# Optimization experiments

Hardware: AMD Instinct MI355X
Metric: run time of the kernel (lower is better)

Reference implementation:

```python
import jax, jax.numpy as jnp
import numpy as np

B, E, C, K, H, OUT = 8192, 16, 256, 2, 64, 387

def setup_inputs() -> dict:
    ks = jax.random.split(jax.random.key(0), 6)
    x = jax.random.normal(ks[0], (B, E, C), dtype=jnp.float32)
    adj = jax.random.normal(ks[1], (E, E), dtype=jnp.float32) * (6.0 / (E + E)) ** 0.5  # xavier-ish
    adj_bias = jax.random.normal(ks[2], (1,), dtype=jnp.float32) * 0.1
    cheb_w = jax.random.normal(ks[3], (K * C, H), dtype=jnp.float32) * (6.0 / (K * C + H)) ** 0.5
    brelu_bias = jnp.zeros((1, 1, H), dtype=jnp.float32)
    fc_w = jax.random.normal(ks[4], (OUT, H), dtype=jnp.float32) * (1.0 / H) ** 0.5
    fc_b = jax.random.normal(ks[5], (OUT,), dtype=jnp.float32) * (1.0 / H) ** 0.5
    return {"x": x, "adj": adj, "adj_bias": adj_bias, "cheb_w": cheb_w,
            "brelu_bias": brelu_bias, "fc_w": fc_w, "fc_b": fc_b}

def reference(x, adj, adj_bias, cheb_w, brelu_bias, fc_w, fc_b):
    # adaptive adjacency + biased ReLU (Eq. 4 prelude)
    w = jax.nn.relu(adj + adj_bias)  # (E,E)
    # normalized Laplacian: I - D^{-1/2} W D^{-1/2}
    d_re = 1.0 / jnp.sqrt(jnp.sum(w, axis=1) + 1e-5)  # (E,)
    lap = jnp.eye(E, dtype=x.dtype) - d_re[:, None] * w * d_re[None, :]  # (E,E)
    # Chebyshev polynomial, k=2: T0 = ones, T1 = lap @ x
    t0 = jnp.ones_like(x)                       # (B,E,C)
    t1 = jnp.einsum('ij,bjc->bic', lap, x)      # (B,E,C)
    # torch: stack on dim=1 -> permute(0,2,3,1) -> flatten(2)  == interleave along last axis
    cp = jnp.stack([t0, t1], axis=-1).reshape(B, E, K * C)  # (B,E,K*C)
    h = jnp.einsum('bek,kh->beh', cp, cheb_w)   # (B,E,H)
    # dropout is identity at eval
    h = jax.nn.relu(brelu_bias + h)
    out = jnp.einsum('beh,oh->beo', h, fc_w) + fc_b  # (B,E,OUT)
    return out
```

## Files before the change

kernel.cpp:

```cpp
#include <hip/hip_runtime.h>
#include <stdint.h>


typedef __attribute__((ext_vector_type(4))) float f32x4;
typedef __attribute__((ext_vector_type(8))) short s16x8;
typedef __attribute__((ext_vector_type(4))) short s16x4;

#define WS_CH_B    0
#define WS_LAP_B   256
#define WS_LAPA_B  1280
#define WS_FCB_B   1792
#define WS_W1T2_B  4096
#define WS_FCW2_B  36864

static __device__ __forceinline__ short f2bf(float f) {
    union { float f; uint32_t u; } v; v.f = f;
    uint32_t r = (v.u + 0x7fffu + ((v.u >> 16) & 1u)) >> 16;
    return (short)r;
}

__global__ void prep_kernel(const float* __restrict__ adj,
                            const float* __restrict__ adj_bias,
                            const float* __restrict__ cheb_w,
                            const float* __restrict__ brelu_bias,
                            const float* __restrict__ fc_w,
                            const float* __restrict__ fc_b,
                            char* __restrict__ ws) {
    float* chf  = (float*)(ws + WS_CH_B);
    float* lapf = (float*)(ws + WS_LAP_B);
    short* lapA = (short*)(ws + WS_LAPA_B);
    float* fcbp = (float*)(ws + WS_FCB_B);
    short* w1t2 = (short*)(ws + WS_W1T2_B);
    short* fcw2 = (short*)(ws + WS_FCW2_B);
    int t = threadIdx.x;

    if (blockIdx.x == 0) {
        __shared__ float sw[16][17];
        __shared__ float sdre[16];
        __shared__ float slap[16][16];
        __shared__ float csum[4][64];
        float ab = adj_bias[0];
        {
            int i = t >> 4, j = t & 15;
            sw[i][j] = fmaxf(adj[t] + ab, 0.f);
        }
        {
            int hh = t & 63, part = t >> 6;
            float s = 0.f;
            #pragma unroll 8
            for (int i = 0; i < 64; ++i) s += cheb_w[(2 * (part * 64 + i)) * 64 + hh];
            csum[part][hh] = s;
        }
        __syncthreads();
        if (t < 16) {
            float s = 0.f;
            #pragma unroll
            for (int j = 0; j < 16; ++j) s += sw[t][j];
            sdre[t] = 1.0f / sqrtf(s + 1e-5f);
        }
        __syncthreads();
        {
            int i = t >> 4, j = t & 15;
            float l = (i == j ? 1.f : 0.f) - sdre[i] * sw[i][j] * sdre[j];
            slap[i][j] = l;
            lapf[t] = l;
        }
        __syncthreads();
        if (t < 64) {
            int m = t & 15, qq = t >> 4;
            #pragma unroll
            for (int i = 0; i < 4; ++i)
                lapA[t * 4 + i] = f2bf(slap[m][qq * 4 + i]);
            chf[t] = csum[0][t] + csum[1][t] + csum[2][t] + csum[3][t] + brelu_bias[t];
        }
        for (int o = t; o < 400; o += 256) fcbp[o] = (o < 387) ? fc_b[o] : 0.f;
    }
    int gt = blockIdx.x * blockDim.x + t;
    int nthr = gridDim.x * blockDim.x;
    for (int idx = gt; idx < 32 * 512; idx += nthr) {
        int frag = idx >> 9, r = idx & 511;
        int lane = r >> 3, j = r & 7;
        int kb = frag >> 2, nt = frag & 3;
        int k = kb * 32 + (lane >> 4) * 8 + j;
        int col = nt * 16 + (lane & 15);
        w1t2[idx] = f2bf(cheb_w[(2 * k + 1) * 64 + col]);
    }
    for (int idx = gt; idx < 50 * 512; idx += nthr) {
        int frag = idx >> 9, r = idx & 511;
        int lane = r >> 3, j = r & 7;
        int tt = frag >> 1, f = frag & 1;
        int o = tt * 16 + (lane & 15);
        int k = f * 32 + (lane >> 4) * 8 + j;
        fcw2[idx] = (o < 387) ? f2bf(fc_w[o * 64 + k]) : (short)0;
    }
}

__global__ __launch_bounds__(256) void fused_kernel(
        const float* __restrict__ x,
        const char* __restrict__ ws,
        float* __restrict__ out) {
    const float* chf  = (const float*)(ws + WS_CH_B);
    const short* lapA = (const short*)(ws + WS_LAPA_B);
    const float* fcbp = (const float*)(ws + WS_FCB_B);
    const short* w1t2 = (const short*)(ws + WS_W1T2_B);
    const short* fcw2 = (const short*)(ws + WS_FCW2_B);

    __shared__ __align__(16) short hs[4][16][72];

    const int lane = threadIdx.x & 63;
    const int wave = threadIdx.x >> 6;
    const int n = lane & 15;
    const int q = lane >> 4;
    const long b = (long)blockIdx.x * 4 + wave;

    const float* xrow = x + b * 4096 + n * 256 + q * 8;
    f32x4 xr[16];
    #pragma unroll
    for (int kb = 0; kb < 8; ++kb) {
        xr[2 * kb]     = *(const f32x4*)(xrow + kb * 32);
        xr[2 * kb + 1] = *(const f32x4*)(xrow + kb * 32 + 4);
    }
    s16x8 af[8];
    #pragma unroll
    for (int kb = 0; kb < 8; ++kb) {
        f32x4 xa = xr[2 * kb], xc = xr[2 * kb + 1];
        af[kb][0] = f2bf(xa[0]); af[kb][1] = f2bf(xa[1]);
        af[kb][2] = f2bf(xa[2]); af[kb][3] = f2bf(xa[3]);
        af[kb][4] = f2bf(xc[0]); af[kb][5] = f2bf(xc[1]);
        af[kb][6] = f2bf(xc[2]); af[kb][7] = f2bf(xc[3]);
    }
    const short* w1 = w1t2 + lane * 8;
    s16x8 bfr[2][4];
    #pragma unroll
    for (int nt = 0; nt < 4; ++nt)
        bfr[0][nt] = *(const s16x8*)(w1 + nt * 512);
    f32x4 g[4];
    #pragma unroll
    for (int nt = 0; nt < 4; ++nt) g[nt] = (f32x4){0.f, 0.f, 0.f, 0.f};
    #pragma unroll
    for (int kb = 0; kb < 8; ++kb) {
        const int cur = kb & 1;
        if (kb < 7) {
            #pragma unroll
            for (int nt = 0; nt < 4; ++nt)
                bfr[cur ^ 1][nt] = *(const s16x8*)(w1 + ((kb + 1) * 4 + nt) * 512);
        }
        #pragma unroll
        for (int nt = 0; nt < 4; ++nt)
            g[nt] = __builtin_amdgcn_mfma_f32_16x16x32_bf16(af[kb], bfr[cur][nt], g[nt], 0, 0, 0);
    }

    f32x4 h[4];
#if defined(__has_builtin) && __has_builtin(__builtin_amdgcn_mfma_f32_16x16x16bf16_1k)
    {
        s16x4 la = *(const s16x4*)(lapA + lane * 4);
        const f32x4 z4 = (f32x4){0.f, 0.f, 0.f, 0.f};
        #pragma unroll
        for (int nt = 0; nt < 4; ++nt) {
            s16x4 gb;
            gb[0] = f2bf(g[nt][0]); gb[1] = f2bf(g[nt][1]);
            gb[2] = f2bf(g[nt][2]); gb[3] = f2bf(g[nt][3]);
            h[nt] = __builtin_amdgcn_mfma_f32_16x16x16bf16_1k(la, gb, z4, 0, 0, 0);
        }
    }
#else
    {
        __shared__ float gs[4][16][68];
        const float* lapf = (const float*)(ws + WS_LAP_B);
        #pragma unroll
        for (int r = 0; r < 4; ++r) {
            gs[wave][q * 4 + r][0 * 16 + n] = g[0][r];
            gs[wave][q * 4 + r][1 * 16 + n] = g[1][r];
            gs[wave][q * 4 + r][2 * 16 + n] = g[2][r];
            gs[wave][q * 4 + r][3 * 16 + n] = g[3][r];
        }
        __syncthreads();
        #pragma unroll
        for (int nt = 0; nt < 4; ++nt) h[nt] = (f32x4){0.f, 0.f, 0.f, 0.f};
        #pragma unroll
        for (int e = 0; e < 16; ++e) {
            float l0 = lapf[(q * 4 + 0) * 16 + e];
            float l1 = lapf[(q * 4 + 1) * 16 + e];
            float l2 = lapf[(q * 4 + 2) * 16 + e];
            float l3 = lapf[(q * 4 + 3) * 16 + e];
            #pragma unroll
            for (int nt = 0; nt < 4; ++nt) {
                float gv = gs[wave][e][nt * 16 + n];
                h[nt][0] += l0 * gv; h[nt][1] += l1 * gv;
                h[nt][2] += l2 * gv; h[nt][3] += l3 * gv;
            }
        }
    }
#endif

    #pragma unroll
    for (int nt = 0; nt < 4; ++nt) {
        float cv = chf[nt * 16 + n];
        #pragma unroll
        for (int r = 0; r < 4; ++r) {
            float v = fmaxf(h[nt][r] + cv, 0.f);
            hs[wave][q * 4 + r][nt * 16 + n] = f2bf(v);
        }
    }
    __builtin_amdgcn_s_waitcnt(0xC07F);

    const short* fw = fcw2 + lane * 8;
    s16x8 fb[2][10];
    #pragma unroll
    for (int t = 0; t < 5; ++t) {
        fb[0][2 * t]     = *(const s16x8*)(fw + (t * 2 + 0) * 512);
        fb[0][2 * t + 1] = *(const s16x8*)(fw + (t * 2 + 1) * 512);
    }
    s16x8 ha0 = *(const s16x8*)(&hs[wave][n][q * 8]);
    s16x8 ha1 = *(const s16x8*)(&hs[wave][n][32 + q * 8]);
    float* outb = out + (b * 16 + q * 4) * 387;
    #pragma unroll
    for (int c = 0; c < 5; ++c) {
        if (c < 4) {
            #pragma unroll
            for (int t = 0; t < 5; ++t) {
                int tt = (c + 1) * 5 + t;
                fb[(c + 1) & 1][2 * t]     = *(const s16x8*)(fw + (tt * 2 + 0) * 512);
                fb[(c + 1) & 1][2 * t + 1] = *(const s16x8*)(fw + (tt * 2 + 1) * 512);
            }
        }
        #pragma unroll
        for (int t = 0; t < 5; ++t) {
            const int tt = c * 5 + t;
            const int o = tt * 16 + n;
            float bias = fcbp[o];
            f32x4 acc = (f32x4){bias, bias, bias, bias};
            acc = __builtin_amdgcn_mfma_f32_16x16x32_bf16(ha0, fb[c & 1][2 * t], acc, 0, 0, 0);
            acc = __builtin_amdgcn_mfma_f32_16x16x32_bf16(ha1, fb[c & 1][2 * t + 1], acc, 0, 0, 0);
            if (o < 387) {
                outb[0 * 387 + o] = acc[0];
                outb[1 * 387 + o] = acc[1];
                outb[2 * 387 + o] = acc[2];
                outb[3 * 387 + o] = acc[3];
            }
        }
    }
}

extern "C" void kernel_launch(void* const* d_in, const int* in_sizes, int n_in,
                              void* d_out, int out_size, void* d_ws, size_t ws_size,
                              hipStream_t stream) {
    const float* x          = (const float*)d_in[0];
    const float* adj        = (const float*)d_in[1];
    const float* adj_bias   = (const float*)d_in[2];
    const float* cheb_w     = (const float*)d_in[3];
    const float* brelu_bias = (const float*)d_in[4];
    const float* fc_w       = (const float*)d_in[5];
    const float* fc_b       = (const float*)d_in[6];
    float* outp = (float*)d_out;
    char* ws = (char*)d_ws;

    prep_kernel<<<64, 256, 0, stream>>>(adj, adj_bias, cheb_w, brelu_bias, fc_w, fc_b, ws);
    fused_kernel<<<2048, 256, 0, stream>>>(x, ws, outp);
}
```

Measured before the change: 345.1 us.

## Stage cheb weights in LDS and split FC output tiles across waves

At the start of the block, the cheb weight fragments (32KB) are copied into shared memory, and the first GEMM reads its B operands from LDS instead of global/L2. The FC stage is also re-partitioned. Each wave now loads only its own subset of output-column tiles of fc_w and applies them to all four waves' hidden rows, which are shared through LDS after a barrier. This cuts per-wave fc_w loads by roughly 4x, at the cost of a block-wide barrier, about 32KB more LDS per block (lower occupancy), and load imbalance because 25 tiles are spread over 4 waves.

Measured after the change: 343.0 us. No clear change (-0.6%).

```diff
diff --git a/kernel.cpp b/kernel.cpp
--- a/kernel.cpp
+++ b/kernel.cpp
@@ -105,13 +105,22 @@
     const short* w1t2 = (const short*)(ws + WS_W1T2_B);
     const short* fcw2 = (const short*)(ws + WS_FCW2_B);
 
-    __shared__ __align__(16) short hs[4][16][72];
+    __shared__ __align__(16) short sw1[32 * 512];
+    __shared__ __align__(16) short hs[4][16][80];
 
     const int lane = threadIdx.x & 63;
     const int wave = threadIdx.x >> 6;
     const int n = lane & 15;
     const int q = lane >> 4;
     const long b = (long)blockIdx.x * 4 + wave;
+
+    {
+        const s16x8* srcv = (const s16x8*)w1t2;
+        s16x8* dstv = (s16x8*)sw1;
+        #pragma unroll
+        for (int i = 0; i < 8; ++i)
+            dstv[i * 256 + threadIdx.x] = srcv[i * 256 + threadIdx.x];
+    }
 
     const float* xrow = x + b * 4096 + n * 256 + q * 8;
     f32x4 xr[16];
@@ -129,11 +138,13 @@
         af[kb][4] = f2bf(xc[0]); af[kb][5] = f2bf(xc[1]);
         af[kb][6] = f2bf(xc[2]); af[kb][7] = f2bf(xc[3]);
     }
-    const short* w1 = w1t2 + lane * 8;
+    __syncthreads();
+
+    const short* w1l = sw1 + lane * 8;
     s16x8 bfr[2][4];
     #pragma unroll
     for (int nt = 0; nt < 4; ++nt)
-        bfr[0][nt] = *(const s16x8*)(w1 + nt * 512);
+        bfr[0][nt] = *(const s16x8*)(w1l + nt * 512);
     f32x4 g[4];
     #pragma unroll
     for (int nt = 0; nt < 4; ++nt) g[nt] = (f32x4){0.f, 0.f, 0.f, 0.f};
@@ -143,7 +154,7 @@
         if (kb < 7) {
             #pragma unroll
             for (int nt = 0; nt < 4; ++nt)
-                bfr[cur ^ 1][nt] = *(const s16x8*)(w1 + ((kb + 1) * 4 + nt) * 512);
+                bfr[cur ^ 1][nt] = *(const s16x8*)(w1l + ((kb + 1) * 4 + nt) * 512);
         }
         #pragma unroll
         for (int nt = 0; nt < 4; ++nt)
@@ -202,37 +213,45 @@
             hs[wave][q * 4 + r][nt * 16 + n] = f2bf(v);
         }
     }
-    __builtin_amdgcn_s_waitcnt(0xC07F);
 
     const short* fw = fcw2 + lane * 8;
-    s16x8 fb[2][10];
-    #pragma unroll
-    for (int t = 0; t < 5; ++t) {
-        fb[0][2 * t]     = *(const s16x8*)(fw + (t * 2 + 0) * 512);
-        fb[0][2 * t + 1] = *(const s16x8*)(fw + (t * 2 + 1) * 512);
-    }
-    s16x8 ha0 = *(const s16x8*)(&hs[wave][n][q * 8]);
-    s16x8 ha1 = *(const s16x8*)(&hs[wave][n][32 + q * 8]);
-    float* outb = out + (b * 16 + q * 4) * 387;
-    #pragma unroll
-    for (int c = 0; c < 5; ++c) {
-        if (c < 4) {
-            #pragma unroll
-            for (int t = 0; t < 5; ++t) {
-                int tt = (c + 1) * 5 + t;
-                fb[(c + 1) & 1][2 * t]     = *(const s16x8*)(fw + (tt * 2 + 0) * 512);
-                fb[(c + 1) & 1][2 * t + 1] = *(const s16x8*)(fw + (tt * 2 + 1) * 512);
-            }
-        }
-        #pragma unroll
-        for (int t = 0; t < 5; ++t) {
-            const int tt = c * 5 + t;
-            const int o = tt * 16 + n;
-            float bias = fcbp[o];
+    s16x8 fb[2][2];
+    {
+        const int tt0 = wave;
+        fb[0][0] = *(const s16x8*)(fw + (tt0 * 2 + 0) * 512);
+        fb[0][1] = *(const s16x8*)(fw + (tt0 * 2 + 1) * 512);
+    }
+    asm volatile("s_waitcnt lgkmcnt(0)" ::: "memory");
+    __builtin_amdgcn_s_barrier();
+    __builtin_amdgcn_sched_barrier(0);
+
+    s16x8 ha[4][2];
+    #pragma unroll
+    for (int gi = 0; gi < 4; ++gi) {
+        ha[gi][0] = *(const s16x8*)(&hs[gi][n][q * 8]);
+        ha[gi][1] = *(const s16x8*)(&hs[gi][n][32 + q * 8]);
+    }
+
+    const long bbase = (long)blockIdx.x * 4;
+    #pragma unroll
+    for (int i = 0; i < 7; ++i) {
+        const int tt = wave + 4 * i;
+        if (tt >= 25) break;
+        const int cur = i & 1;
+        const int tn = tt + 4;
+        if (tn < 25) {
+            fb[cur ^ 1][0] = *(const s16x8*)(fw + (tn * 2 + 0) * 512);
+            fb[cur ^ 1][1] = *(const s16x8*)(fw + (tn * 2 + 1) * 512);
+        }
+        const int o = tt * 16 + n;
+        const float bias = fcbp[o];
+        #pragma unroll
+        for (int gi = 0; gi < 4; ++gi) {
             f32x4 acc = (f32x4){bias, bias, bias, bias};
-            acc = __builtin_amdgcn_mfma_f32_16x16x32_bf16(ha0, fb[c & 1][2 * t], acc, 0, 0, 0);
-            acc = __builtin_amdgcn_mfma_f32_16x16x32_bf16(ha1, fb[c & 1][2 * t + 1], acc, 0, 0, 0);
+            acc = __builtin_amdgcn_mfma_f32_16x16x32_bf16(ha[gi][0], fb[cur][0], acc, 0, 0, 0);
+            acc = __builtin_amdgcn_mfma_f32_16x16x32_bf16(ha[gi][1], fb[cur][1], acc, 0, 0, 0);
             if (o < 387) {
+                float* outb = out + ((bbase + gi) * 16 + q * 4) * 387;
                 outb[0 * 387 + o] = acc[0];
                 outb[1 * 387 + o] = acc[1];
                 outb[2 * 387 + o] = acc[2];
```
